# Performance work log

Measured on AMD Instinct MI355X. Metric: run time of the kernel, lower is better.

## Reference

```python
import jax, jax.numpy as jnp
import numpy as np

B, Q, K, H = 16, 512, 512, 64
DQ, DK, DV = 256, 256, 256
MASK_VAL = -1000000.0


def setup_inputs() -> dict:
    key = jax.random.key(0)
    ks = jax.random.split(key, 7)
    queries = jax.random.normal(ks[0], (B, Q, DQ), dtype=jnp.float32)
    keys = jax.random.normal(ks[1], (B, K, DK), dtype=jnp.float32)
    values = jax.random.normal(ks[2], (B, K, DV), dtype=jnp.float32)
    valid_lens = jax.random.randint(ks[3], (B,), 1, K + 1).astype(jnp.int32)
    # learned params (nn.Linear, bias=False): weight shape [out, in]
    Wq = jax.random.normal(ks[4], (H, DQ), dtype=jnp.float32) / np.sqrt(DQ)
    Wk = jax.random.normal(ks[5], (H, DK), dtype=jnp.float32) / np.sqrt(DK)
    wv = jax.random.normal(ks[6], (H,), dtype=jnp.float32) / np.sqrt(H)
    return {"queries": queries, "keys": keys, "values": values,
            "valid_lens": valid_lens, "Wq": Wq, "Wk": Wk, "wv": wv}


def reference(queries, keys, values, valid_lens, Wq, Wk, wv):
    q = jnp.einsum('bqd,hd->bqh', queries, Wq)          # [B,Q,H]
    k = jnp.einsum('bkd,hd->bkh', keys, Wk)             # [B,K,H]
    feats = jnp.tanh(q[:, :, None, :] + k[:, None, :, :])  # [B,Q,K,H]
    scores = jnp.einsum('bqkh,h->bqk', feats, wv)       # [B,Q,K]
    kmask = jnp.arange(K)[None, None, :] < valid_lens[:, None, None]
    scores = jnp.where(kmask, scores, MASK_VAL)
    attn = jax.nn.softmax(scores, axis=-1)              # [B,Q,K]
    return jnp.einsum('bqk,bkv->bqv', attn, values)     # [B,Q,DV]
```

## Files before the change

### kernel.cpp

```cpp
#include <hip/hip_runtime.h>
#include <math.h>

#if defined(__has_builtin)
#  if __has_builtin(__builtin_amdgcn_exp2f)
#    define EXP2F(x) __builtin_amdgcn_exp2f(x)
#  endif
#  if __has_builtin(__builtin_amdgcn_rcpf)
#    define RCPF(x) __builtin_amdgcn_rcpf(x)
#  endif
#endif
#ifndef EXP2F
#  define EXP2F(x) exp2f(x)
#endif
#ifndef RCPF
#  define RCPF(x) (1.0f/(x))
#endif

static constexpr int Bn = 16, QN = 512, KN = 512, Hn = 64, DV = 256, DIN = 256;
static constexpr int TQ = 8;
static constexpr float TWO_LOG2E = 2.8853900817779268f;
static constexpr float LOG2E     = 1.4426950408889634f;

__global__ __launch_bounds__(256) void proj_kernel(
    const float* __restrict__ X, const float* __restrict__ W,
    float* __restrict__ out, int transposed)
{
  __shared__ __align__(16) float xs[DIN];
  __shared__ __align__(16) float red[Hn * 4];
  int row = blockIdx.x;
  int t = threadIdx.x;
  xs[t] = X[(size_t)row * DIN + t];
  __syncthreads();
  int h = t >> 2, part = t & 3;
  const float* wrow = W + h * DIN;
  float acc = 0.f;
  #pragma unroll
  for (int j = 0; j < 16; ++j) {
    int i = part * 4 + j * 16;
    float4 w4 = *(const float4*)(wrow + i);
    float4 x4 = *(const float4*)(xs + i);
    acc += w4.x * x4.x + w4.y * x4.y + w4.z * x4.z + w4.w * x4.w;
  }
  red[h * 4 + part] = acc;
  __syncthreads();
  if (t < Hn) {
    float4 r4 = *(const float4*)(red + t * 4);
    float s = r4.x + r4.y + r4.z + r4.w;
    int b = row >> 9, r = row & (QN - 1);
    if (transposed) out[((size_t)b * Hn + t) * KN + r] = s;
    else            out[(size_t)row * Hn + t] = s;
  }
}

__global__ __launch_bounds__(256) void attn_kernel(
    const float* __restrict__ qproj,
    const float* __restrict__ kprojT,
    const float* __restrict__ values,
    const int*   __restrict__ valid_lens,
    const float* __restrict__ wv,
    float* __restrict__ out)
{
  __shared__ __align__(16) float qe[TQ * Hn];
  __shared__ __align__(16) float wv2[Hn];
  __shared__ __align__(16) float pt[KN][12];
  __shared__ float inv_s[TQ];

  int t = threadIdx.x;
  int b = blockIdx.x >> 6;
  int q0 = (blockIdx.x & 63) * TQ;
  int L = valid_lens[b];

  {
    const float* qp = qproj + ((size_t)b * QN + q0) * Hn;
    qe[t]       = EXP2F(qp[t]       * TWO_LOG2E);
    qe[t + 256] = EXP2F(qp[t + 256] * TWO_LOG2E);
  }
  if (t < Hn) wv2[t] = 2.0f * wv[t];
  __syncthreads();

  float S = 0.f;
  #pragma unroll 8
  for (int h = 0; h < Hn; ++h) S += wv2[h];
  S *= 0.5f;

  const float* kp = kprojT + (size_t)b * Hn * KN;
  #pragma unroll
  for (int kk = 0; kk < 2; ++kk) {
    int k = t + kk * 256;
    if (k < L) {
      float acc[TQ];
      #pragma unroll
      for (int r = 0; r < TQ; ++r) acc[r] = S;
      #pragma unroll 4
      for (int h = 0; h < Hn; ++h) {
        float kv = kp[(size_t)h * KN + k];
        float ek = EXP2F(kv * TWO_LOG2E);
        float w2 = wv2[h];
        #pragma unroll
        for (int r = 0; r < TQ; ++r) {
          float d = qe[r * Hn + h] * ek + 1.0f;
          acc[r] -= w2 * RCPF(d);
        }
      }
      *(float4*)&pt[k][0] = make_float4(acc[0], acc[1], acc[2], acc[3]);
      *(float4*)&pt[k][4] = make_float4(acc[4], acc[5], acc[6], acc[7]);
    }
  }
  __syncthreads();

  int lane = t & 63, wave = t >> 6;
  #pragma unroll
  for (int rr = 0; rr < 2; ++rr) {
    int r = wave + rr * 4;
    float sv[8];
    float m = -3.0e38f;
    #pragma unroll
    for (int j = 0; j < 8; ++j) {
      int k = lane + j * 64;
      sv[j] = (k < L) ? pt[k][r] : -3.0e38f;
      m = fmaxf(m, sv[j]);
    }
    #pragma unroll
    for (int off = 32; off > 0; off >>= 1) m = fmaxf(m, __shfl_xor(m, off, 64));
    float sum = 0.f;
    #pragma unroll
    for (int j = 0; j < 8; ++j) {
      int k = lane + j * 64;
      if (k < L) {
        float p = EXP2F((sv[j] - m) * LOG2E);
        pt[k][r] = p;
        sum += p;
      }
    }
    #pragma unroll
    for (int off = 32; off > 0; off >>= 1) sum += __shfl_xor(sum, off, 64);
    if (lane == 0) inv_s[r] = 1.0f / sum;
  }
  __syncthreads();

  float acc[TQ];
  #pragma unroll
  for (int r = 0; r < TQ; ++r) acc[r] = 0.f;
  const float* vb = values + (size_t)b * KN * DV + t;
  #pragma unroll 4
  for (int k = 0; k < L; ++k) {
    float val = vb[(size_t)k * DV];
    float4 pa = *(const float4*)&pt[k][0];
    float4 pb = *(const float4*)&pt[k][4];
    acc[0] += pa.x * val; acc[1] += pa.y * val;
    acc[2] += pa.z * val; acc[3] += pa.w * val;
    acc[4] += pb.x * val; acc[5] += pb.y * val;
    acc[6] += pb.z * val; acc[7] += pb.w * val;
  }
  float* ob = out + ((size_t)b * QN + q0) * DV + t;
  #pragma unroll
  for (int r = 0; r < TQ; ++r) ob[(size_t)r * DV] = acc[r] * inv_s[r];
}

extern "C" void kernel_launch(void* const* d_in, const int* in_sizes, int n_in,
                              void* d_out, int out_size, void* d_ws, size_t ws_size,
                              hipStream_t stream) {
  const float* queries    = (const float*)d_in[0];
  const float* keys       = (const float*)d_in[1];
  const float* values     = (const float*)d_in[2];
  const int*   valid_lens = (const int*)d_in[3];
  const float* Wq         = (const float*)d_in[4];
  const float* Wk         = (const float*)d_in[5];
  const float* wv         = (const float*)d_in[6];
  float* out = (float*)d_out;

  float* qproj  = (float*)d_ws;
  float* kprojT = qproj + (size_t)Bn * QN * Hn;

  proj_kernel<<<Bn * QN, 256, 0, stream>>>(queries, Wq, qproj, 0);
  proj_kernel<<<Bn * KN, 256, 0, stream>>>(keys,    Wk, kprojT, 1);
  attn_kernel<<<Bn * (QN / TQ), 256, 0, stream>>>(qproj, kprojT, values,
                                                  valid_lens, wv, out);
}
```

Measured before the change: 178.1 us.

## Tile and merge projection kernels, precompute exps, split attention PV over halves

The two projection launches are merged into one 512-block kernel that tiles 32 rows per block through shared memory and stores exp(2x) of the projections, so the attention kernel no longer recomputes exponentials per query tile. The attention kernel moves to 512 threads with one key per thread. It drops the max-subtraction pass of the softmax (scores are bounded by the wv sum) and reduces row sums through per-wave partials. The P·V loop is split across two thread halves over k, combined through shared memory, and blocks are reordered to interleave batches. Skipping the max subtraction relies on scores staying small enough for exp not to overflow, and the extra pacc buffer adds shared memory.

Result: faster. 156.9 us (-11.9%).

```diff
diff --git a/kernel.cpp b/kernel.cpp
--- a/kernel.cpp
+++ b/kernel.cpp
@@ -18,132 +18,143 @@
 
 static constexpr int Bn = 16, QN = 512, KN = 512, Hn = 64, DV = 256, DIN = 256;
 static constexpr int TQ = 8;
+static constexpr int PR = 32;
 static constexpr float TWO_LOG2E = 2.8853900817779268f;
 static constexpr float LOG2E     = 1.4426950408889634f;
 
 __global__ __launch_bounds__(256) void proj_kernel(
-    const float* __restrict__ X, const float* __restrict__ W,
-    float* __restrict__ out, int transposed)
+    const float* __restrict__ queries, const float* __restrict__ keys,
+    const float* __restrict__ Wq, const float* __restrict__ Wk,
+    float* __restrict__ qe, float* __restrict__ ekT)
 {
-  __shared__ __align__(16) float xs[DIN];
-  __shared__ __align__(16) float red[Hn * 4];
-  int row = blockIdx.x;
+  __shared__ __align__(16) float xs[PR][36];
+  int blk = blockIdx.x;
+  bool is_k = blk >= 256;
+  int tile = is_k ? blk - 256 : blk;
+  const float* X = is_k ? keys : queries;
+  const float* W = is_k ? Wk : Wq;
+  int row0 = tile * PR;
   int t = threadIdx.x;
-  xs[t] = X[(size_t)row * DIN + t];
-  __syncthreads();
-  int h = t >> 2, part = t & 3;
-  const float* wrow = W + h * DIN;
-  float acc = 0.f;
+  int c = t & 63;
+  int wg = t >> 6;
+  float acc[8];
   #pragma unroll
-  for (int j = 0; j < 16; ++j) {
-    int i = part * 4 + j * 16;
-    float4 w4 = *(const float4*)(wrow + i);
-    float4 x4 = *(const float4*)(xs + i);
-    acc += w4.x * x4.x + w4.y * x4.y + w4.z * x4.z + w4.w * x4.w;
+  for (int i = 0; i < 8; ++i) acc[i] = 0.f;
+
+  for (int dc = 0; dc < DIN; dc += 32) {
+    __syncthreads();
+    {
+      int row = t >> 3, dp = t & 7;
+      float4 v = *(const float4*)(X + (size_t)(row0 + row) * DIN + dc + dp * 4);
+      *(float4*)&xs[row][dp * 4] = v;
+    }
+    __syncthreads();
+    const float* wr = W + c * DIN + dc;
+    #pragma unroll
+    for (int dd = 0; dd < 32; dd += 4) {
+      float4 w4 = *(const float4*)(wr + dd);
+      #pragma unroll
+      for (int i = 0; i < 8; ++i) {
+        float4 x4 = *(const float4*)&xs[wg * 8 + i][dd];
+        acc[i] += w4.x * x4.x + w4.y * x4.y + w4.z * x4.z + w4.w * x4.w;
+      }
+    }
   }
-  red[h * 4 + part] = acc;
-  __syncthreads();
-  if (t < Hn) {
-    float4 r4 = *(const float4*)(red + t * 4);
-    float s = r4.x + r4.y + r4.z + r4.w;
-    int b = row >> 9, r = row & (QN - 1);
-    if (transposed) out[((size_t)b * Hn + t) * KN + r] = s;
-    else            out[(size_t)row * Hn + t] = s;
+  #pragma unroll
+  for (int i = 0; i < 8; ++i) {
+    int row = row0 + wg * 8 + i;
+    float e = EXP2F(acc[i] * TWO_LOG2E);
+    if (!is_k) {
+      qe[(size_t)row * Hn + c] = e;
+    } else {
+      int b = row >> 9, k = row & (KN - 1);
+      ekT[((size_t)b * Hn + c) * KN + k] = e;
+    }
   }
 }
 
-__global__ __launch_bounds__(256) void attn_kernel(
-    const float* __restrict__ qproj,
-    const float* __restrict__ kprojT,
+__global__ __launch_bounds__(512) void attn_kernel(
+    const float* __restrict__ qe,
+    const float* __restrict__ ekT,
     const float* __restrict__ values,
     const int*   __restrict__ valid_lens,
     const float* __restrict__ wv,
     float* __restrict__ out)
 {
-  __shared__ __align__(16) float qe[TQ * Hn];
-  __shared__ __align__(16) float wv2[Hn];
+  __shared__ __align__(16) float qes[TQ * Hn];
+  __shared__ float wv2[Hn];
   __shared__ __align__(16) float pt[KN][12];
+  __shared__ float wsum[8][8];
   __shared__ float inv_s[TQ];
+  __shared__ __align__(16) float pacc[TQ][DV];
 
   int t = threadIdx.x;
-  int b = blockIdx.x >> 6;
-  int q0 = (blockIdx.x & 63) * TQ;
+  int b = blockIdx.x & 15;
+  int q0 = (blockIdx.x >> 4) * TQ;
   int L = valid_lens[b];
+  int lane = t & 63, wave = t >> 6;
 
-  {
-    const float* qp = qproj + ((size_t)b * QN + q0) * Hn;
-    qe[t]       = EXP2F(qp[t]       * TWO_LOG2E);
-    qe[t + 256] = EXP2F(qp[t + 256] * TWO_LOG2E);
-  }
+  qes[t] = qe[((size_t)b * QN + q0) * Hn + t];
   if (t < Hn) wv2[t] = 2.0f * wv[t];
   __syncthreads();
 
   float S = 0.f;
-  #pragma unroll 8
+  #pragma unroll
   for (int h = 0; h < Hn; ++h) S += wv2[h];
   S *= 0.5f;
 
-  const float* kp = kprojT + (size_t)b * Hn * KN;
-  #pragma unroll
-  for (int kk = 0; kk < 2; ++kk) {
-    int k = t + kk * 256;
+  {
+    int k = t;
+    float sc[TQ];
+    #pragma unroll
+    for (int r = 0; r < TQ; ++r) sc[r] = S;
     if (k < L) {
-      float acc[TQ];
-      #pragma unroll
-      for (int r = 0; r < TQ; ++r) acc[r] = S;
+      const float* kp = ekT + (size_t)b * Hn * KN + k;
       #pragma unroll 4
       for (int h = 0; h < Hn; ++h) {
-        float kv = kp[(size_t)h * KN + k];
-        float ek = EXP2F(kv * TWO_LOG2E);
+        float ek = kp[(size_t)h * KN];
         float w2 = wv2[h];
         #pragma unroll
         for (int r = 0; r < TQ; ++r) {
-          float d = qe[r * Hn + h] * ek + 1.0f;
-          acc[r] -= w2 * RCPF(d);
+          float d = qes[r * Hn + h] * ek + 1.0f;
+          sc[r] -= w2 * RCPF(d);
         }
       }
-      *(float4*)&pt[k][0] = make_float4(acc[0], acc[1], acc[2], acc[3]);
-      *(float4*)&pt[k][4] = make_float4(acc[4], acc[5], acc[6], acc[7]);
+    }
+    float p[TQ];
+    #pragma unroll
+    for (int r = 0; r < TQ; ++r) p[r] = (k < L) ? EXP2F(sc[r] * LOG2E) : 0.f;
+    if (k < L) {
+      *(float4*)&pt[k][0] = make_float4(p[0], p[1], p[2], p[3]);
+      *(float4*)&pt[k][4] = make_float4(p[4], p[5], p[6], p[7]);
+    }
+    #pragma unroll
+    for (int r = 0; r < TQ; ++r) {
+      float s = p[r];
+      #pragma unroll
+      for (int off = 32; off > 0; off >>= 1) s += __shfl_xor(s, off, 64);
+      if (lane == r) wsum[wave][r] = s;
     }
   }
   __syncthreads();
-
-  int lane = t & 63, wave = t >> 6;
-  #pragma unroll
-  for (int rr = 0; rr < 2; ++rr) {
-    int r = wave + rr * 4;
-    float sv[8];
-    float m = -3.0e38f;
+  if (t < TQ) {
+    float s = 0.f;
     #pragma unroll
-    for (int j = 0; j < 8; ++j) {
-      int k = lane + j * 64;
-      sv[j] = (k < L) ? pt[k][r] : -3.0e38f;
-      m = fmaxf(m, sv[j]);
-    }
-    #pragma unroll
-    for (int off = 32; off > 0; off >>= 1) m = fmaxf(m, __shfl_xor(m, off, 64));
-    float sum = 0.f;
-    #pragma unroll
-    for (int j = 0; j < 8; ++j) {
-      int k = lane + j * 64;
-      if (k < L) {
-        float p = EXP2F((sv[j] - m) * LOG2E);
-        pt[k][r] = p;
-        sum += p;
-      }
-    }
-    #pragma unroll
-    for (int off = 32; off > 0; off >>= 1) sum += __shfl_xor(sum, off, 64);
-    if (lane == 0) inv_s[r] = 1.0f / sum;
+    for (int w = 0; w < 8; ++w) s += wsum[w][t];
+    inv_s[t] = 1.0f / s;
   }
   __syncthreads();
 
+  int col = t & (DV - 1), half = t >> 8;
+  int mid = L >> 1;
+  int k0 = half ? mid : 0;
+  int k1 = half ? L : mid;
   float acc[TQ];
   #pragma unroll
   for (int r = 0; r < TQ; ++r) acc[r] = 0.f;
-  const float* vb = values + (size_t)b * KN * DV + t;
+  const float* vb = values + (size_t)b * KN * DV + col;
   #pragma unroll 4
-  for (int k = 0; k < L; ++k) {
+  for (int k = k0; k < k1; ++k) {
     float val = vb[(size_t)k * DV];
     float4 pa = *(const float4*)&pt[k][0];
     float4 pb = *(const float4*)&pt[k][4];
@@ -152,9 +163,17 @@
     acc[4] += pb.x * val; acc[5] += pb.y * val;
     acc[6] += pb.z * val; acc[7] += pb.w * val;
   }
-  float* ob = out + ((size_t)b * QN + q0) * DV + t;
-  #pragma unroll
-  for (int r = 0; r < TQ; ++r) ob[(size_t)r * DV] = acc[r] * inv_s[r];
+  if (half) {
+    #pragma unroll
+    for (int r = 0; r < TQ; ++r) pacc[r][col] = acc[r];
+  }
+  __syncthreads();
+  if (!half) {
+    float* ob = out + ((size_t)b * QN + q0) * DV + col;
+    #pragma unroll
+    for (int r = 0; r < TQ; ++r)
+      ob[(size_t)r * DV] = (acc[r] + pacc[r][col]) * inv_s[r];
+  }
 }
 
 extern "C" void kernel_launch(void* const* d_in, const int* in_sizes, int n_in,
@@ -169,11 +188,10 @@
   const float* wv         = (const float*)d_in[6];
   float* out = (float*)d_out;
 
-  float* qproj  = (float*)d_ws;
-  float* kprojT = qproj + (size_t)Bn * QN * Hn;
+  float* qe  = (float*)d_ws;
+  float* ekT = qe + (size_t)Bn * QN * Hn;
 
-  proj_kernel<<<Bn * QN, 256, 0, stream>>>(queries, Wq, qproj, 0);
-  proj_kernel<<<Bn * KN, 256, 0, stream>>>(keys,    Wk, kprojT, 1);
-  attn_kernel<<<Bn * (QN / TQ), 256, 0, stream>>>(qproj, kprojT, values,
+  proj_kernel<<<512, 256, 0, stream>>>(queries, keys, Wq, Wk, qe, ekT);
+  attn_kernel<<<Bn * (QN / TQ), 512, 0, stream>>>(qe, ekT, values,
                                                   valid_lens, wv, out);
 }
```
